# Kernel optimization log

Measured on AMD Instinct MI355X. Metric: run time of the kernel, lower is better.

The kernel has to match this reference:

```python
import jax, jax.numpy as jnp
import numpy as np

N_NODES = 100000
N_EDGES = 1600000
IN_DIM = 64
HID = 64
EDGE_DIM = 1
NUM_GRAPHS = 1000
SCALE = 0.05


def setup_inputs() -> dict:
    key = jax.random.key(0)
    ks = jax.random.split(key, 20)
    x = jax.random.normal(ks[0], (N_NODES, IN_DIM), dtype=jnp.float32)
    edge_index = jax.random.randint(ks[1], (2, N_EDGES), 0, N_NODES, dtype=jnp.int64)
    edge_attr = jax.random.normal(ks[2], (N_EDGES, EDGE_DIM), dtype=jnp.float32)
    batch = jnp.sort(jax.random.randint(ks[3], (N_NODES,), 0, NUM_GRAPHS, dtype=jnp.int64))
    p = lambda k, shp: SCALE * jax.random.normal(k, shp, dtype=jnp.float32)
    return {
        "x": x, "edge_index": edge_index, "edge_attr": edge_attr, "batch": batch,
        # conv1 MLP + edge lin
        "W1a": p(ks[4], (IN_DIM, HID)), "b1a": p(ks[5], (HID,)),
        "W1b": p(ks[6], (HID, HID)), "b1b": p(ks[7], (HID,)),
        "We1": p(ks[8], (EDGE_DIM, IN_DIM)), "be1": p(ks[9], (IN_DIM,)),
        # conv2 MLP + edge lin
        "W2a": p(ks[10], (HID, HID)), "b2a": p(ks[11], (HID,)),
        "W2b": p(ks[12], (HID, HID)), "b2b": p(ks[13], (HID,)),
        "We2": p(ks[14], (EDGE_DIM, HID)), "be2": p(ks[15], (HID,)),
        # classifier
        "Wc1": p(ks[16], (HID, HID)), "bc1": p(ks[17], (HID,)),
        "Wc2": p(ks[18], (HID, 1)), "bc2": p(ks[19], (1,)),
    }


def _gine(x, src, dst, e_proj, Wa, ba, Wb, bb):
    # message: ReLU(x_src + projected edge feature); scatter-sum to target
    msg = jax.nn.relu(x[src] + e_proj)                      # [E, D]
    agg = jax.ops.segment_sum(msg, dst, num_segments=x.shape[0])
    h = x + agg                                             # eps = 0 (default)
    return jax.nn.relu(h @ Wa + ba) @ Wb + bb               # GIN MLP


def reference(x, edge_index, edge_attr, batch,
              W1a, b1a, W1b, b1b, We1, be1,
              W2a, b2a, W2b, b2b, We2, be2,
              Wc1, bc1, Wc2, bc2):
    src, dst = edge_index[0], edge_index[1]
    h = _gine(x, src, dst, edge_attr @ We1 + be1, W1a, b1a, W1b, b1b)
    h = jax.nn.relu(h)  # dropout is identity in eval mode
    h = _gine(h, src, dst, edge_attr @ We2 + be2, W2a, b2a, W2b, b2b)
    h = jax.nn.relu(h)
    # global mean pool over graphs
    sums = jax.ops.segment_sum(h, batch, num_segments=NUM_GRAPHS)
    cnts = jax.ops.segment_sum(jnp.ones((h.shape[0], 1), h.dtype), batch, num_segments=NUM_GRAPHS)
    pooled = sums / jnp.maximum(cnts, 1.0)                  # [G, HID]
    return jax.nn.relu(pooled @ Wc1 + bc1) @ Wc2 + bc2      # [G, 1]
```

## Files before the change

### kernel.cpp

```cpp
#include <hip/hip_runtime.h>

#define N_NODES    100000
#define N_EDGES    1600000
#define DIM        64
#define NUM_GRAPHS 1000
#define PAD        72

#define SLICES     512
#define SLICE_E    3125
#define NBUCK      782
#define CAP4       3072
#define HIST_BLK   256

typedef __attribute__((ext_vector_type(8))) short bf16x8;
typedef __attribute__((ext_vector_type(4))) float f32x4;

__device__ __forceinline__ unsigned short f2bf(float f) {
    unsigned int b = __float_as_uint(f);
    b += 0x7FFFu + ((b >> 16) & 1u);
    return (unsigned short)(b >> 16);
}

__device__ __forceinline__ float4 ntload_f4(const float* p) {
    f32x4 v = __builtin_nontemporal_load((const f32x4*)p);
    return make_float4(v.x, v.y, v.z, v.w);
}

__global__ __launch_bounds__(256) void prep_hist(
    const int* __restrict__ ei, int* __restrict__ bucketTotal)
{
    __shared__ int lh[NBUCK];
    int blk = blockIdx.x, t = threadIdx.x;
    for (int i = t; i < NBUCK; i += 256) lh[i] = 0;
    __syncthreads();
    const int* dsts = ei + N_EDGES + blk * (2 * SLICE_E);
    for (int k = t; k < 2 * SLICE_E; k += 256)
        atomicAdd(&lh[dsts[k] >> 7], 1);
    __syncthreads();
    for (int i = t; i < NBUCK; i += 256) {
        int h = lh[i];
        if (h) atomicAdd(&bucketTotal[i], h);
    }
}

__global__ __launch_bounds__(1024) void csr_c2a(
    const int* __restrict__ bucketTotal, int* __restrict__ bucketStart,
    int* __restrict__ cursor)
{
    __shared__ int sc[1024];
    int t = threadIdx.x;
    int v = (t < NBUCK) ? bucketTotal[t] : 0;
    sc[t] = v;
    __syncthreads();
    for (int o = 1; o < 1024; o <<= 1) {
        int u = (t >= o) ? sc[t - o] : 0;
        __syncthreads();
        sc[t] += u;
        __syncthreads();
    }
    if (t < NBUCK) {
        int e = sc[t] - v;
        bucketStart[t] = e;
        cursor[t] = e;
    }
    if (t == NBUCK - 1) bucketStart[NBUCK] = sc[t];
}

__global__ __launch_bounds__(512) void csr_build(
    const int* __restrict__ ei, const float* __restrict__ ea,
    const float* __restrict__ x,
    int* __restrict__ cursor, int2* __restrict__ tmp,
    unsigned short* __restrict__ x16)
{
    __shared__ int2 staging[SLICE_E];
    __shared__ int  lh[NBUCK];
    __shared__ int  lstart[NBUCK + 1];
    __shared__ int  garr[NBUCK];
    __shared__ unsigned short barr[SLICE_E];
    __shared__ int  part[512];

    int s = blockIdx.x, t = threadIdx.x;
    const int* dsts = ei + N_EDGES + s * SLICE_E;

    for (int i = t; i < NBUCK; i += 512) lh[i] = 0;
    __syncthreads();
    for (int k = t; k < SLICE_E; k += 512)
        atomicAdd(&lh[dsts[k] >> 7], 1);

    {
        int gid = s * 512 + t;
        for (int it = gid; it < N_NODES * DIM / 8; it += SLICES * 512) {
            int base = it * 8;
            float4 f0 = ntload_f4(x + base);
            float4 f1 = ntload_f4(x + base + 4);
            uint4 o;
            o.x = (unsigned)f2bf(f0.x) | ((unsigned)f2bf(f0.y) << 16);
            o.y = (unsigned)f2bf(f0.z) | ((unsigned)f2bf(f0.w) << 16);
            o.z = (unsigned)f2bf(f1.x) | ((unsigned)f2bf(f1.y) << 16);
            o.w = (unsigned)f2bf(f1.z) | ((unsigned)f2bf(f1.w) << 16);
            *(uint4*)(x16 + base) = o;
        }
    }
    __syncthreads();

    int h[2];
    int mysum = 0;
    #pragma unroll
    for (int j = 0; j < 2; ++j) {
        int b = 2 * t + j;
        h[j] = (b < NBUCK) ? lh[b] : 0;
        mysum += h[j];
    }
    part[t] = mysum;
    __syncthreads();
    for (int o = 1; o < 512; o <<= 1) {
        int u = (t >= o) ? part[t - o] : 0;
        __syncthreads();
        part[t] += u;
        __syncthreads();
    }
    int run = part[t] - mysum;
    #pragma unroll
    for (int j = 0; j < 2; ++j) {
        int b = 2 * t + j;
        if (b < NBUCK) {
            lstart[b] = run;
            if (h[j]) garr[b] = atomicAdd(&cursor[b], h[j]);
        }
        run += h[j];
    }
    if (t == 0) lstart[NBUCK] = SLICE_E;
    __syncthreads();

    for (int i = t; i < NBUCK; i += 512) lh[i] = 0;
    #pragma unroll
    for (int j = 0; j < 2; ++j) {
        int b = 2 * t + j;
        if (b < NBUCK)
            for (int i = lstart[b]; i < lstart[b + 1]; ++i)
                barr[i] = (unsigned short)b;
    }
    __syncthreads();

    for (int k = t; k < SLICE_E; k += 512) {
        int e   = s * SLICE_E + k;
        int src = ei[e];
        int dst = dsts[k];
        float a = ea[e];
        int b   = dst >> 7;
        int p   = lstart[b] + atomicAdd(&lh[b], 1);
        staging[p] = make_int2(((dst & 127) << 17) | src, __float_as_int(a));
    }
    __syncthreads();

    for (int i = t; i < SLICE_E; i += 512) {
        int b = barr[i];
        tmp[garr[b] + (i - lstart[b])] = staging[i];
    }
}

__global__ __launch_bounds__(512, 6) void gine_sort(
    const uint2* __restrict__ g2,
    const float* __restrict__ self32,
    const int*   __restrict__ bucketStart,
    const int2*  __restrict__ tmp,
    int2* __restrict__ csr_e,
    int*  __restrict__ rowptr,
    const float* __restrict__ We, const float* __restrict__ be,
    const float* __restrict__ Wa, const float* __restrict__ ba,
    const float* __restrict__ Wb, const float* __restrict__ bb,
    unsigned int* __restrict__ out16)
{
    __shared__ int2 staging[CAP4];
    __shared__ int  nh[128];
    __shared__ int  nscan[128];
    __shared__ int  ncur[128];
    __shared__ short sWat[64 * PAD];
    __shared__ short sWbt[64 * PAD];
    __shared__ short h16[32 * PAD];
    __shared__ short t16[32 * PAD];

    int t = threadIdx.x;
    int b = blockIdx.x;
    int lo = bucketStart[b], hi = bucketStart[b + 1];
    int cnt = hi - lo;
    int node0 = b << 7;
    int nn = min(128, N_NODES - node0);

    for (int i = t; i < 4096; i += 512) {
        int k = i >> 6, n = i & 63;
        sWat[n * PAD + k] = (short)f2bf(Wa[i]);
        sWbt[n * PAD + k] = (short)f2bf(Wb[i]);
    }
    if (t < 128) { nh[t] = 0; ncur[t] = 0; }
    __syncthreads();

    int2 r[6];
    int nr = 0;
    for (int k = t; k < cnt; k += 512) {
        int2 v = tmp[lo + k];
        r[nr++] = v;
        atomicAdd(&nh[v.x >> 17], 1);
    }
    __syncthreads();

    if (t < 128) nscan[t] = nh[t];
    __syncthreads();
    for (int o = 1; o < 128; o <<= 1) {
        int u = (t >= o && t < 128) ? nscan[t - o] : 0;
        __syncthreads();
        if (t < 128) nscan[t] += u;
        __syncthreads();
    }
    if (t < 128) nscan[t] -= nh[t];
    __syncthreads();

    if (t < nn) rowptr[node0 + t] = lo + nscan[t];
    if (b == NBUCK - 1 && t == 0) rowptr[N_NODES] = N_EDGES;

    for (int k = 0; k < nr; ++k) {
        int dl = r[k].x >> 17;
        int p  = nscan[dl] + atomicAdd(&ncur[dl], 1);
        staging[p] = r[k];
    }
    __syncthreads();

    for (int i = t; i < cnt; i += 512) {
        int2 v = staging[i];
        csr_e[lo + i] = make_int2((v.x & 0x1FFFF) << 4, v.y);
    }

    int wave = t >> 6;
    int lane = t & 63;
    int quad = lane >> 4;
    int l15  = lane & 15;
    int slot = wave * 4 + quad;
    int d0   = l15 * 4;
    float4 wp = *(const float4*)(We + d0);
    float4 bp = *(const float4*)(be + d0);
    int mtile = wave & 1;
    int ntile = wave >> 1;
    int col   = ntile * 16 + l15;
    int am    = mtile * 16 + l15;
    float bav = ba[col], bbv = bb[col];
    int cclamp = max(cnt - 1, 0);
    __syncthreads();

    for (int g = 0; g < 4; ++g) {
        int  lrow  = g * 32 + slot;
        bool valid = lrow < nn;
        int deg = valid ? nh[lrow] : 0;
        int beg = valid ? min(nscan[lrow], cclamp) : 0;
        int dm = deg;
        dm = max(dm, __shfl_xor(dm, 16));
        dm = max(dm, __shfl_xor(dm, 32));

        float4 agg = make_float4(0.f, 0.f, 0.f, 0.f);
        #define EDGE4(rr, uu, cond)                                              \
        {                                                                        \
            float s = (cond) ? 1.f : 0.f, av = __int_as_float(rr.y);             \
            float e0 = __uint_as_float(uu.x << 16);                              \
            float e1 = __uint_as_float(uu.x & 0xFFFF0000u);                      \
            float e2 = __uint_as_float(uu.y << 16);                              \
            float e3 = __uint_as_float(uu.y & 0xFFFF0000u);                      \
            agg.x = fmaf(s, fmaxf(e0 + fmaf(av, wp.x, bp.x), 0.f), agg.x);       \
            agg.y = fmaf(s, fmaxf(e1 + fmaf(av, wp.y, bp.y), 0.f), agg.y);       \
            agg.z = fmaf(s, fmaxf(e2 + fmaf(av, wp.z, bp.z), 0.f), agg.z);       \
            agg.w = fmaf(s, fmaxf(e3 + fmaf(av, wp.w, bp.w), 0.f), agg.w);       \
        }
        for (int j = 0; j < dm; j += 4) {
            int2 r0 = staging[beg + ((j + 0) < deg ? j + 0 : 0)];
            int2 r1 = staging[beg + ((j + 1) < deg ? j + 1 : 0)];
            int2 r2 = staging[beg + ((j + 2) < deg ? j + 2 : 0)];
            int2 r3 = staging[beg + ((j + 3) < deg ? j + 3 : 0)];
            uint2 u0 = g2[(r0.x & 0x1FFFF) * 16 + l15];
            uint2 u1 = g2[(r1.x & 0x1FFFF) * 16 + l15];
            uint2 u2 = g2[(r2.x & 0x1FFFF) * 16 + l15];
            uint2 u3 = g2[(r3.x & 0x1FFFF) * 16 + l15];
            EDGE4(r0, u0, (j + 0) < deg)
            EDGE4(r1, u1, (j + 1) < deg)
            EDGE4(r2, u2, (j + 2) < deg)
            EDGE4(r3, u3, (j + 3) < deg)
        }
        #undef EDGE4
        if (valid) {
            float4 sv = *(const float4*)(self32 + (size_t)(node0 + lrow) * DIM + d0);
            agg.x += sv.x; agg.y += sv.y; agg.z += sv.z; agg.w += sv.w;
        }
        {
            unsigned lov = (unsigned)f2bf(agg.x) | ((unsigned)f2bf(agg.y) << 16);
            unsigned hiv = (unsigned)f2bf(agg.z) | ((unsigned)f2bf(agg.w) << 16);
            *(uint2*)&h16[slot * PAD + d0] = make_uint2(lov, hiv);
        }
        __syncthreads();

        f32x4 acc = {bav, bav, bav, bav};
        #pragma unroll
        for (int s = 0; s < 2; ++s) {
            bf16x8 a = *(const bf16x8*)&h16[am * PAD + s * 32 + quad * 8];
            bf16x8 bb8 = *(const bf16x8*)&sWat[col * PAD + s * 32 + quad * 8];
            acc = __builtin_amdgcn_mfma_f32_16x16x32_bf16(a, bb8, acc, 0, 0, 0);
        }
        #pragma unroll
        for (int rr = 0; rr < 4; ++rr) {
            int row = mtile * 16 + quad * 4 + rr;
            t16[row * PAD + col] = (short)f2bf(fmaxf(acc[rr], 0.f));
        }
        __syncthreads();

        f32x4 acc2 = {bbv, bbv, bbv, bbv};
        #pragma unroll
        for (int s = 0; s < 2; ++s) {
            bf16x8 a = *(const bf16x8*)&t16[am * PAD + s * 32 + quad * 8];
            bf16x8 bb8 = *(const bf16x8*)&sWbt[col * PAD + s * 32 + quad * 8];
            acc2 = __builtin_amdgcn_mfma_f32_16x16x32_bf16(a, bb8, acc2, 0, 0, 0);
        }
        #pragma unroll
        for (int rr = 0; rr < 4; ++rr) {
            int row = mtile * 16 + quad * 4 + rr;
            h16[row * PAD + col] = (short)f2bf(fmaxf(acc2[rr], 0.f));
        }
        __syncthreads();
        {
            int n2 = t >> 4, dd = (t & 15) * 2;
            int lnode = g * 32 + n2;
            if (node0 + lnode < N_NODES) {
                uint2 v = *(const uint2*)&h16[n2 * PAD + dd * 2];
                *(uint2*)&out16[(size_t)(node0 + lnode) * 32 + dd] = v;
            }
        }
        __syncthreads();
    }
}

template<bool SELF32>
__global__ __launch_bounds__(512, 8) void gine_mfma(
    const uint2* __restrict__ g2,
    const float* __restrict__ self32,
    const int*   __restrict__ rowptr,
    const int2*  __restrict__ csr_e,
    const float* __restrict__ We, const float* __restrict__ be,
    const float* __restrict__ Wa, const float* __restrict__ ba,
    const float* __restrict__ Wb, const float* __restrict__ bb,
    unsigned int* __restrict__ out16)
{
    __shared__ short sWat[64 * PAD];
    __shared__ short sWbt[64 * PAD];
    __shared__ short h16[32 * PAD];
    __shared__ short t16[32 * PAD];

    int t = threadIdx.x;
    for (int i = t; i < 4096; i += 512) {
        int k = i >> 6, n = i & 63;
        sWat[n * PAD + k] = (short)f2bf(Wa[i]);
        sWbt[n * PAD + k] = (short)f2bf(Wb[i]);
    }
    int wave = t >> 6;
    int lane = t & 63;
    int quad = lane >> 4;
    int l15  = lane & 15;
    int slot = wave * 4 + quad;
    int d0   = l15 * 4;
    float4 wp = *(const float4*)(We + d0);
    float4 bp = *(const float4*)(be + d0);
    int mtile = wave & 1;
    int ntile = wave >> 1;
    int col   = ntile * 16 + l15;
    int am    = mtile * 16 + l15;
    float bav = ba[col], bbv = bb[col];
    __syncthreads();

    for (int base = blockIdx.x * 32; base < N_NODES; base += gridDim.x * 32) {
        int  node  = base + slot;
        bool valid = node < N_NODES;
        int beg = 0, deg = 0;
        if (valid) {
            beg = rowptr[node];
            deg = rowptr[node + 1] - beg;
            beg = min(beg, N_EDGES - 1);
        }
        int dm = deg;
        dm = max(dm, __shfl_xor(dm, 16));
        dm = max(dm, __shfl_xor(dm, 32));

        float4 agg = make_float4(0.f, 0.f, 0.f, 0.f);
        #define EDGE4(rr, uu, cond)                                              \
        {                                                                        \
            float s = (cond) ? 1.f : 0.f, av = __int_as_float(rr.y);             \
            float e0 = __uint_as_float(uu.x << 16);                              \
            float e1 = __uint_as_float(uu.x & 0xFFFF0000u);                      \
            float e2 = __uint_as_float(uu.y << 16);                              \
            float e3 = __uint_as_float(uu.y & 0xFFFF0000u);                      \
            agg.x = fmaf(s, fmaxf(e0 + fmaf(av, wp.x, bp.x), 0.f), agg.x);       \
            agg.y = fmaf(s, fmaxf(e1 + fmaf(av, wp.y, bp.y), 0.f), agg.y);       \
            agg.z = fmaf(s, fmaxf(e2 + fmaf(av, wp.z, bp.z), 0.f), agg.z);       \
            agg.w = fmaf(s, fmaxf(e3 + fmaf(av, wp.w, bp.w), 0.f), agg.w);       \
        }
        for (int j = 0; j < dm; j += 4) {
            int2 r0 = csr_e[beg + ((j + 0) < deg ? j + 0 : 0)];
            int2 r1 = csr_e[beg + ((j + 1) < deg ? j + 1 : 0)];
            int2 r2 = csr_e[beg + ((j + 2) < deg ? j + 2 : 0)];
            int2 r3 = csr_e[beg + ((j + 3) < deg ? j + 3 : 0)];
            uint2 u0 = g2[r0.x + l15];
            uint2 u1 = g2[r1.x + l15];
            uint2 u2 = g2[r2.x + l15];
            uint2 u3 = g2[r3.x + l15];
            EDGE4(r0, u0, (j + 0) < deg)
            EDGE4(r1, u1, (j + 1) < deg)
            EDGE4(r2, u2, (j + 2) < deg)
            EDGE4(r3, u3, (j + 3) < deg)
        }
        #undef EDGE4
        if (valid) {
            if (SELF32) {
                float4 sv = *(const float4*)(self32 + (size_t)node * DIM + d0);
                agg.x += sv.x; agg.y += sv.y; agg.z += sv.z; agg.w += sv.w;
            } else {
                uint2 u = g2[node * 16 + l15];
                agg.x += __uint_as_float(u.x << 16);
                agg.y += __uint_as_float(u.x & 0xFFFF0000u);
                agg.z += __uint_as_float(u.y << 16);
                agg.w += __uint_as_float(u.y & 0xFFFF0000u);
            }
        }
        {
            unsigned lo = (unsigned)f2bf(agg.x) | ((unsigned)f2bf(agg.y) << 16);
            unsigned hi = (unsigned)f2bf(agg.z) | ((unsigned)f2bf(agg.w) << 16);
            *(uint2*)&h16[slot * PAD + d0] = make_uint2(lo, hi);
        }
        __syncthreads();

        f32x4 acc = {bav, bav, bav, bav};
        #pragma unroll
        for (int s = 0; s < 2; ++s) {
            bf16x8 a = *(const bf16x8*)&h16[am * PAD + s * 32 + quad * 8];
            bf16x8 b = *(const bf16x8*)&sWat[col * PAD + s * 32 + quad * 8];
            acc = __builtin_amdgcn_mfma_f32_16x16x32_bf16(a, b, acc, 0, 0, 0);
        }
        #pragma unroll
        for (int r = 0; r < 4; ++r) {
            int row = mtile * 16 + quad * 4 + r;
            t16[row * PAD + col] = (short)f2bf(fmaxf(acc[r], 0.f));
        }
        __syncthreads();

        f32x4 acc2 = {bbv, bbv, bbv, bbv};
        #pragma unroll
        for (int s = 0; s < 2; ++s) {
            bf16x8 a = *(const bf16x8*)&t16[am * PAD + s * 32 + quad * 8];
            bf16x8 b = *(const bf16x8*)&sWbt[col * PAD + s * 32 + quad * 8];
            acc2 = __builtin_amdgcn_mfma_f32_16x16x32_bf16(a, b, acc2, 0, 0, 0);
        }
        #pragma unroll
        for (int r = 0; r < 4; ++r) {
            int row = mtile * 16 + quad * 4 + r;
            h16[row * PAD + col] = (short)f2bf(fmaxf(acc2[r], 0.f));
        }
        __syncthreads();
        {
            int nn = t >> 4, dd = (t & 15) * 2;
            if (base + nn < N_NODES) {
                uint2 v = *(const uint2*)&h16[nn * PAD + dd * 2];
                *(uint2*)&out16[(size_t)(base + nn) * 32 + dd] = v;
            }
        }
        __syncthreads();
    }
}

__device__ __forceinline__ int lbound(const int* __restrict__ a, int key) {
    int lo = 0, hi = N_NODES;
    while (lo < hi) {
        int mid = (lo + hi) >> 1;
        if (a[mid] < key) lo = mid + 1; else hi = mid;
    }
    return lo;
}

__global__ __launch_bounds__(256) void pool_cls(
    const unsigned int* __restrict__ B16b,
    const int* __restrict__ batch,
    const float* __restrict__ Wc1,  const float* __restrict__ bc1,
    const float* __restrict__ Wc2,  const float* __restrict__ bc2,
    float* __restrict__ out)
{
    __shared__ float sW[64 * 64];
    __shared__ float sp[4][64];

    int t = threadIdx.x;
    for (int i = t; i < 64 * 64; i += 256) sW[i] = Wc1[i];

    int nl   = t >> 6;
    int lane = t & 63;
    int g    = blockIdx.x * 4 + nl;

    int p = lane & 31, h = lane >> 5;
    if (g < NUM_GRAPHS) {
        int s = lbound(batch, g);
        int e = lbound(batch, g + 1);
        float2 sum = make_float2(0.f, 0.f);
        for (int i = s + h; i < e; i += 2) {
            unsigned u = B16b[(size_t)i * 32 + p];
            sum.x += __uint_as_float(u << 16);
            sum.y += __uint_as_float(u & 0xFFFF0000u);
        }
        sum.x += __shfl_xor(sum.x, 32);
        sum.y += __shfl_xor(sum.y, 32);
        if (h == 0) {
            float inv = 1.f / (float)max(e - s, 1);
            sp[nl][2 * p]     = sum.x * inv;
            sp[nl][2 * p + 1] = sum.y * inv;
        }
    } else if (h == 0) {
        sp[nl][2 * p] = 0.f;
        sp[nl][2 * p + 1] = 0.f;
    }
    __syncthreads();

    float acc = bc1[lane];
    #pragma unroll
    for (int k = 0; k < 64; ++k)
        acc = fmaf(sp[nl][k], sW[k * 64 + lane], acc);
    float tv = fmaxf(acc, 0.f) * Wc2[lane];

    #pragma unroll
    for (int off = 32; off > 0; off >>= 1)
        tv += __shfl_down(tv, off);

    if (lane == 0 && g < NUM_GRAPHS) out[g] = tv + bc2[0];
}

extern "C" void kernel_launch(void* const* d_in, const int* in_sizes, int n_in,
                              void* d_out, int out_size, void* d_ws, size_t ws_size,
                              hipStream_t stream) {
    const float* x     = (const float*)d_in[0];
    const int*   ei    = (const int*)  d_in[1];
    const float* ea    = (const float*)d_in[2];
    const int*   batch = (const int*)  d_in[3];
    const float* W1a = (const float*)d_in[4];
    const float* b1a = (const float*)d_in[5];
    const float* W1b = (const float*)d_in[6];
    const float* b1b = (const float*)d_in[7];
    const float* We1 = (const float*)d_in[8];
    const float* be1 = (const float*)d_in[9];
    const float* W2a = (const float*)d_in[10];
    const float* b2a = (const float*)d_in[11];
    const float* W2b = (const float*)d_in[12];
    const float* b2b = (const float*)d_in[13];
    const float* We2 = (const float*)d_in[14];
    const float* be2 = (const float*)d_in[15];
    const float* Wc1 = (const float*)d_in[16];
    const float* bc1 = (const float*)d_in[17];
    const float* Wc2 = (const float*)d_in[18];
    const float* bc2 = (const float*)d_in[19];

    int2*           csr_e  = (int2*)d_ws;
    unsigned short* x16    = (unsigned short*)(csr_e + N_EDGES);
    unsigned short* B16    = x16 + (size_t)N_NODES * DIM;
    unsigned short* B16b   = B16 + (size_t)N_NODES * DIM;
    int2*           tmp    = (int2*)B16b;
    int*            bucketTotal = (int*)(B16b + (size_t)N_NODES * DIM);
    int*            bucketStart = bucketTotal + NBUCK;
    int*            cursor = bucketStart + (NBUCK + 1);
    int*            rowptr = cursor + NBUCK;

    hipMemsetAsync(bucketTotal, 0, NBUCK * sizeof(int), stream);

    prep_hist<<<HIST_BLK, 256, 0, stream>>>(ei, bucketTotal);
    csr_c2a<<<1, 1024, 0, stream>>>(bucketTotal, bucketStart, cursor);
    csr_build<<<SLICES, 512, 0, stream>>>(ei, ea, x, cursor, tmp, x16);

    gine_sort<<<NBUCK, 512, 0, stream>>>(
        (const uint2*)x16, x, bucketStart, tmp, csr_e, rowptr,
        We1, be1, W1a, b1a, W1b, b1b, (unsigned int*)B16);

    gine_mfma<false><<<1024, 512, 0, stream>>>(
        (const uint2*)B16, nullptr, rowptr, csr_e,
        We2, be2, W2a, b2a, W2b, b2b, (unsigned int*)B16b);

    pool_cls<<<(NUM_GRAPHS + 3) / 4, 256, 0, stream>>>(
        (const unsigned int*)B16b, batch, Wc1, bc1, Wc2, bc2, (float*)d_out);
}
```

Before: 316.4 us.

## Fuse histogram pass into CSR build and gather per-slice segments in sort

New measurement: 307.7 us. 2.7% less time.

```diff
diff --git a/kernel.cpp b/kernel.cpp
--- a/kernel.cpp
+++ b/kernel.cpp
@@ -10,7 +10,7 @@
 #define SLICE_E    3125
 #define NBUCK      782
 #define CAP4       3072
-#define HIST_BLK   256
+#define LROW       (NBUCK + 1)
 
 typedef __attribute__((ext_vector_type(8))) short bf16x8;
 typedef __attribute__((ext_vector_type(4))) float f32x4;
@@ -26,66 +26,37 @@
     return make_float4(v.x, v.y, v.z, v.w);
 }
 
-__global__ __launch_bounds__(256) void prep_hist(
-    const int* __restrict__ ei, int* __restrict__ bucketTotal)
-{
-    __shared__ int lh[NBUCK];
-    int blk = blockIdx.x, t = threadIdx.x;
-    for (int i = t; i < NBUCK; i += 256) lh[i] = 0;
-    __syncthreads();
-    const int* dsts = ei + N_EDGES + blk * (2 * SLICE_E);
-    for (int k = t; k < 2 * SLICE_E; k += 256)
-        atomicAdd(&lh[dsts[k] >> 7], 1);
-    __syncthreads();
-    for (int i = t; i < NBUCK; i += 256) {
-        int h = lh[i];
-        if (h) atomicAdd(&bucketTotal[i], h);
-    }
-}
-
-__global__ __launch_bounds__(1024) void csr_c2a(
-    const int* __restrict__ bucketTotal, int* __restrict__ bucketStart,
-    int* __restrict__ cursor)
-{
-    __shared__ int sc[1024];
-    int t = threadIdx.x;
-    int v = (t < NBUCK) ? bucketTotal[t] : 0;
-    sc[t] = v;
-    __syncthreads();
-    for (int o = 1; o < 1024; o <<= 1) {
-        int u = (t >= o) ? sc[t - o] : 0;
-        __syncthreads();
-        sc[t] += u;
-        __syncthreads();
-    }
-    if (t < NBUCK) {
-        int e = sc[t] - v;
-        bucketStart[t] = e;
-        cursor[t] = e;
-    }
-    if (t == NBUCK - 1) bucketStart[NBUCK] = sc[t];
-}
-
-__global__ __launch_bounds__(512) void csr_build(
+__global__ __launch_bounds__(512) void fused_build(
     const int* __restrict__ ei, const float* __restrict__ ea,
     const float* __restrict__ x,
-    int* __restrict__ cursor, int2* __restrict__ tmp,
-    unsigned short* __restrict__ x16)
+    int* __restrict__ bucketTotal, int* __restrict__ lstartG,
+    int2* __restrict__ tmp, unsigned short* __restrict__ x16)
 {
     __shared__ int2 staging[SLICE_E];
     __shared__ int  lh[NBUCK];
-    __shared__ int  lstart[NBUCK + 1];
-    __shared__ int  garr[NBUCK];
-    __shared__ unsigned short barr[SLICE_E];
+    __shared__ int  lst[NBUCK + 1];
     __shared__ int  part[512];
 
     int s = blockIdx.x, t = threadIdx.x;
-    const int* dsts = ei + N_EDGES + s * SLICE_E;
+    const int*   srcs = ei + s * SLICE_E;
+    const int*   dsts = ei + N_EDGES + s * SLICE_E;
+    const float* eas  = ea + s * SLICE_E;
 
     for (int i = t; i < NBUCK; i += 512) lh[i] = 0;
     __syncthreads();
-    for (int k = t; k < SLICE_E; k += 512)
-        atomicAdd(&lh[dsts[k] >> 7], 1);
+
+    int2  r[7];
+    short rb[7];
+    int nr = 0;
+    for (int k = t; k < SLICE_E; k += 512) {
+        int src = srcs[k], dst = dsts[k];
+        float a = eas[k];
+        int b = dst >> 7;
+        r[nr]  = make_int2(((dst & 127) << 17) | src, __float_as_int(a));
+        rb[nr] = (short)b;
+        ++nr;
+        atomicAdd(&lh[b], 1);
+    }
 
     {
         int gid = s * 512 + t;
@@ -124,45 +95,52 @@
     for (int j = 0; j < 2; ++j) {
         int b = 2 * t + j;
         if (b < NBUCK) {
-            lstart[b] = run;
-            if (h[j]) garr[b] = atomicAdd(&cursor[b], h[j]);
+            lst[b] = run;
+            if (h[j]) atomicAdd(&bucketTotal[b], h[j]);
         }
         run += h[j];
     }
-    if (t == 0) lstart[NBUCK] = SLICE_E;
-    __syncthreads();
-
+    if (t == 0) lst[NBUCK] = SLICE_E;
+    __syncthreads();
+
+    for (int i = t; i <= NBUCK; i += 512) lstartG[s * LROW + i] = lst[i];
     for (int i = t; i < NBUCK; i += 512) lh[i] = 0;
-    #pragma unroll
-    for (int j = 0; j < 2; ++j) {
-        int b = 2 * t + j;
-        if (b < NBUCK)
-            for (int i = lstart[b]; i < lstart[b + 1]; ++i)
-                barr[i] = (unsigned short)b;
-    }
-    __syncthreads();
-
-    for (int k = t; k < SLICE_E; k += 512) {
-        int e   = s * SLICE_E + k;
-        int src = ei[e];
-        int dst = dsts[k];
-        float a = ea[e];
-        int b   = dst >> 7;
-        int p   = lstart[b] + atomicAdd(&lh[b], 1);
-        staging[p] = make_int2(((dst & 127) << 17) | src, __float_as_int(a));
-    }
-    __syncthreads();
-
-    for (int i = t; i < SLICE_E; i += 512) {
-        int b = barr[i];
-        tmp[garr[b] + (i - lstart[b])] = staging[i];
-    }
+    __syncthreads();
+
+    for (int k = 0; k < nr; ++k) {
+        int b = rb[k];
+        int p = lst[b] + atomicAdd(&lh[b], 1);
+        staging[p] = r[k];
+    }
+    __syncthreads();
+
+    int2* out = tmp + s * SLICE_E;
+    for (int i = t; i < SLICE_E; i += 512) out[i] = staging[i];
+}
+
+__global__ __launch_bounds__(1024) void csr_c2a(
+    const int* __restrict__ bucketTotal, int* __restrict__ bucketStart)
+{
+    __shared__ int sc[1024];
+    int t = threadIdx.x;
+    int v = (t < NBUCK) ? bucketTotal[t] : 0;
+    sc[t] = v;
+    __syncthreads();
+    for (int o = 1; o < 1024; o <<= 1) {
+        int u = (t >= o) ? sc[t - o] : 0;
+        __syncthreads();
+        sc[t] += u;
+        __syncthreads();
+    }
+    if (t < NBUCK) bucketStart[t] = sc[t] - v;
+    if (t == NBUCK - 1) bucketStart[NBUCK] = sc[t];
 }
 
 __global__ __launch_bounds__(512, 6) void gine_sort(
     const uint2* __restrict__ g2,
     const float* __restrict__ self32,
     const int*   __restrict__ bucketStart,
+    const int*   __restrict__ lstartG,
     const int2*  __restrict__ tmp,
     int2* __restrict__ csr_e,
     int*  __restrict__ rowptr,
@@ -175,6 +153,7 @@
     __shared__ int  nh[128];
     __shared__ int  nscan[128];
     __shared__ int  ncur[128];
+    __shared__ int  part[512];
     __shared__ short sWat[64 * PAD];
     __shared__ short sWbt[64 * PAD];
     __shared__ short h16[32 * PAD];
@@ -182,8 +161,7 @@
 
     int t = threadIdx.x;
     int b = blockIdx.x;
-    int lo = bucketStart[b], hi = bucketStart[b + 1];
-    int cnt = hi - lo;
+    int lo = bucketStart[b];
     int node0 = b << 7;
     int nn = min(128, N_NODES - node0);
 
@@ -193,31 +171,48 @@
         sWbt[n * PAD + k] = (short)f2bf(Wb[i]);
     }
     if (t < 128) { nh[t] = 0; ncur[t] = 0; }
-    __syncthreads();
+
+    int ls  = lstartG[t * LROW + b];
+    int le  = lstartG[t * LROW + b + 1];
+    int h_s = le - ls;
+    part[t] = h_s;
+    __syncthreads();
+    for (int o = 1; o < 512; o <<= 1) {
+        int u = (t >= o) ? part[t - o] : 0;
+        __syncthreads();
+        part[t] += u;
+        __syncthreads();
+    }
+    int myoff = part[t] - h_s;
+    int cnt   = part[511];
+    {
+        const int2* tsrc = tmp + t * SLICE_E + ls;
+        for (int j = 0; j < h_s; ++j) {
+            int2 v = tsrc[j];
+            staging[myoff + j] = v;
+            atomicAdd(&nh[v.x >> 17], 1);
+        }
+    }
+    __syncthreads();
+
+    if (t < 128) nscan[t] = nh[t];
+    __syncthreads();
+    for (int o = 1; o < 128; o <<= 1) {
+        int u = (t >= o && t < 128) ? nscan[t - o] : 0;
+        __syncthreads();
+        if (t < 128) nscan[t] += u;
+        __syncthreads();
+    }
+    if (t < 128) nscan[t] -= nh[t];
+    __syncthreads();
+
+    if (t < nn) rowptr[node0 + t] = lo + nscan[t];
+    if (b == NBUCK - 1 && t == 0) rowptr[N_NODES] = N_EDGES;
 
     int2 r[6];
     int nr = 0;
-    for (int k = t; k < cnt; k += 512) {
-        int2 v = tmp[lo + k];
-        r[nr++] = v;
-        atomicAdd(&nh[v.x >> 17], 1);
-    }
-    __syncthreads();
-
-    if (t < 128) nscan[t] = nh[t];
-    __syncthreads();
-    for (int o = 1; o < 128; o <<= 1) {
-        int u = (t >= o && t < 128) ? nscan[t - o] : 0;
-        __syncthreads();
-        if (t < 128) nscan[t] += u;
-        __syncthreads();
-    }
-    if (t < 128) nscan[t] -= nh[t];
-    __syncthreads();
-
-    if (t < nn) rowptr[node0 + t] = lo + nscan[t];
-    if (b == NBUCK - 1 && t == 0) rowptr[N_NODES] = N_EDGES;
-
+    for (int k = t; k < cnt; k += 512) r[nr++] = staging[k];
+    __syncthreads();
     for (int k = 0; k < nr; ++k) {
         int dl = r[k].x >> 17;
         int p  = nscan[dl] + atomicAdd(&ncur[dl], 1);
@@ -559,19 +554,18 @@
     unsigned short* B16    = x16 + (size_t)N_NODES * DIM;
     unsigned short* B16b   = B16 + (size_t)N_NODES * DIM;
     int2*           tmp    = (int2*)B16b;
-    int*            bucketTotal = (int*)(B16b + (size_t)N_NODES * DIM);
+    int*            lstartG = (int*)(B16b + (size_t)N_NODES * DIM);
+    int*            bucketTotal = lstartG + SLICES * LROW;
     int*            bucketStart = bucketTotal + NBUCK;
-    int*            cursor = bucketStart + (NBUCK + 1);
-    int*            rowptr = cursor + NBUCK;
+    int*            rowptr = bucketStart + (NBUCK + 1);
 
     hipMemsetAsync(bucketTotal, 0, NBUCK * sizeof(int), stream);
 
-    prep_hist<<<HIST_BLK, 256, 0, stream>>>(ei, bucketTotal);
-    csr_c2a<<<1, 1024, 0, stream>>>(bucketTotal, bucketStart, cursor);
-    csr_build<<<SLICES, 512, 0, stream>>>(ei, ea, x, cursor, tmp, x16);
+    fused_build<<<SLICES, 512, 0, stream>>>(ei, ea, x, bucketTotal, lstartG, tmp, x16);
+    csr_c2a<<<1, 1024, 0, stream>>>(bucketTotal, bucketStart);
 
     gine_sort<<<NBUCK, 512, 0, stream>>>(
-        (const uint2*)x16, x, bucketStart, tmp, csr_e, rowptr,
+        (const uint2*)x16, x, bucketStart, lstartG, tmp, csr_e, rowptr,
         We1, be1, W1a, b1a, W1b, b1b, (unsigned int*)B16);
 
     gine_mfma<false><<<1024, 512, 0, stream>>>(
```

## Move x-to-bf16 conversion into histogram kernel and cache edges in registers

Applied to the files above, without the earlier changes.

New measurement: 317.5 us. No clear change (+0.3%).

```diff
diff --git a/kernel.cpp b/kernel.cpp
--- a/kernel.cpp
+++ b/kernel.cpp
@@ -4,13 +4,13 @@
 #define N_EDGES    1600000
 #define DIM        64
 #define NUM_GRAPHS 1000
+#define CONV_BLK   3125
 #define PAD        72
 
 #define SLICES     512
 #define SLICE_E    3125
 #define NBUCK      782
 #define CAP4       3072
-#define HIST_BLK   256
 
 typedef __attribute__((ext_vector_type(8))) short bf16x8;
 typedef __attribute__((ext_vector_type(4))) float f32x4;
@@ -26,20 +26,36 @@
     return make_float4(v.x, v.y, v.z, v.w);
 }
 
-__global__ __launch_bounds__(256) void prep_hist(
-    const int* __restrict__ ei, int* __restrict__ bucketTotal)
+__global__ __launch_bounds__(256) void prep(
+    const int* __restrict__ ei, const float* __restrict__ x,
+    int* __restrict__ bucketTotal, unsigned short* __restrict__ x16)
 {
     __shared__ int lh[NBUCK];
     int blk = blockIdx.x, t = threadIdx.x;
-    for (int i = t; i < NBUCK; i += 256) lh[i] = 0;
-    __syncthreads();
-    const int* dsts = ei + N_EDGES + blk * (2 * SLICE_E);
-    for (int k = t; k < 2 * SLICE_E; k += 256)
-        atomicAdd(&lh[dsts[k] >> 7], 1);
-    __syncthreads();
-    for (int i = t; i < NBUCK; i += 256) {
-        int h = lh[i];
-        if (h) atomicAdd(&bucketTotal[i], h);
+    if (blk < SLICES) {
+        for (int i = t; i < NBUCK; i += 256) lh[i] = 0;
+        __syncthreads();
+        const int* dsts = ei + N_EDGES + blk * SLICE_E;
+        for (int k = t; k < SLICE_E; k += 256)
+            atomicAdd(&lh[dsts[k] >> 7], 1);
+        __syncthreads();
+        for (int i = t; i < NBUCK; i += 256) {
+            int h = lh[i];
+            if (h) atomicAdd(&bucketTotal[i], h);
+        }
+    } else {
+        int tt = (blk - SLICES) * 256 + t;
+        if (tt < N_NODES * DIM / 8) {
+            int base = tt * 8;
+            float4 f0 = ntload_f4(x + base);
+            float4 f1 = ntload_f4(x + base + 4);
+            uint4 o;
+            o.x = (unsigned)f2bf(f0.x) | ((unsigned)f2bf(f0.y) << 16);
+            o.y = (unsigned)f2bf(f0.z) | ((unsigned)f2bf(f0.w) << 16);
+            o.z = (unsigned)f2bf(f1.x) | ((unsigned)f2bf(f1.y) << 16);
+            o.w = (unsigned)f2bf(f1.z) | ((unsigned)f2bf(f1.w) << 16);
+            *(uint4*)(x16 + base) = o;
+        }
     }
 }
 
@@ -66,11 +82,9 @@
     if (t == NBUCK - 1) bucketStart[NBUCK] = sc[t];
 }
 
-__global__ __launch_bounds__(512) void csr_build(
+__global__ __launch_bounds__(512) void csr_c3(
     const int* __restrict__ ei, const float* __restrict__ ea,
-    const float* __restrict__ x,
-    int* __restrict__ cursor, int2* __restrict__ tmp,
-    unsigned short* __restrict__ x16)
+    int* __restrict__ cursor, int2* __restrict__ tmp)
 {
     __shared__ int2 staging[SLICE_E];
     __shared__ int  lh[NBUCK];
@@ -80,26 +94,24 @@
     __shared__ int  part[512];
 
     int s = blockIdx.x, t = threadIdx.x;
-    const int* dsts = ei + N_EDGES + s * SLICE_E;
+    const int*   srcs = ei + s * SLICE_E;
+    const int*   dsts = ei + N_EDGES + s * SLICE_E;
+    const float* eas  = ea + s * SLICE_E;
 
     for (int i = t; i < NBUCK; i += 512) lh[i] = 0;
     __syncthreads();
-    for (int k = t; k < SLICE_E; k += 512)
-        atomicAdd(&lh[dsts[k] >> 7], 1);
-
-    {
-        int gid = s * 512 + t;
-        for (int it = gid; it < N_NODES * DIM / 8; it += SLICES * 512) {
-            int base = it * 8;
-            float4 f0 = ntload_f4(x + base);
-            float4 f1 = ntload_f4(x + base + 4);
-            uint4 o;
-            o.x = (unsigned)f2bf(f0.x) | ((unsigned)f2bf(f0.y) << 16);
-            o.y = (unsigned)f2bf(f0.z) | ((unsigned)f2bf(f0.w) << 16);
-            o.z = (unsigned)f2bf(f1.x) | ((unsigned)f2bf(f1.y) << 16);
-            o.w = (unsigned)f2bf(f1.z) | ((unsigned)f2bf(f1.w) << 16);
-            *(uint4*)(x16 + base) = o;
-        }
+
+    int2  r[7];
+    short rb[7];
+    int nr = 0;
+    for (int k = t; k < SLICE_E; k += 512) {
+        int src = srcs[k], dst = dsts[k];
+        float a = eas[k];
+        int b = dst >> 7;
+        r[nr]  = make_int2(((dst & 127) << 17) | src, __float_as_int(a));
+        rb[nr] = (short)b;
+        ++nr;
+        atomicAdd(&lh[b], 1);
     }
     __syncthreads();
 
@@ -142,14 +154,10 @@
     }
     __syncthreads();
 
-    for (int k = t; k < SLICE_E; k += 512) {
-        int e   = s * SLICE_E + k;
-        int src = ei[e];
-        int dst = dsts[k];
-        float a = ea[e];
-        int b   = dst >> 7;
-        int p   = lstart[b] + atomicAdd(&lh[b], 1);
-        staging[p] = make_int2(((dst & 127) << 17) | src, __float_as_int(a));
+    for (int k = 0; k < nr; ++k) {
+        int b = rb[k];
+        int p = lstart[b] + atomicAdd(&lh[b], 1);
+        staging[p] = r[k];
     }
     __syncthreads();
 
@@ -566,9 +574,9 @@
 
     hipMemsetAsync(bucketTotal, 0, NBUCK * sizeof(int), stream);
 
-    prep_hist<<<HIST_BLK, 256, 0, stream>>>(ei, bucketTotal);
+    prep<<<SLICES + CONV_BLK, 256, 0, stream>>>(ei, x, bucketTotal, x16);
     csr_c2a<<<1, 1024, 0, stream>>>(bucketTotal, bucketStart, cursor);
-    csr_build<<<SLICES, 512, 0, stream>>>(ei, ea, x, cursor, tmp, x16);
+    csr_c3<<<SLICES, 512, 0, stream>>>(ei, ea, cursor, tmp);
 
     gine_sort<<<NBUCK, 512, 0, stream>>>(
         (const uint2*)x16, x, bucketStart, tmp, csr_e, rowptr,
```
